# Performance work log

Hardware: AMD Instinct MI355X
Metric: run time of the kernel (lower is better)

## Reference

```python
import jax, jax.numpy as jnp
import numpy as np

N = 50000      # nodes
E = 800000     # edges (avg degree 16)
NF = 128       # input feature dim
H = 128        # hidden dim
GAMMA = 1.0    # gm init arg
COS_EPS = 1e-8 # F.cosine_similarity eps
EW_MIN = 1e-4  # edge-weight clamp


def setup_inputs() -> dict:
    key = jax.random.key(0)
    ks = jax.random.split(key, 9)
    x = jax.random.normal(ks[0], (N, NF), dtype=jnp.float32)
    edge_index = jax.random.randint(ks[1], (2, E), 0, N, dtype=jnp.int64)
    sensitive_attr = jax.random.randint(ks[2], (N,), 0, 2, dtype=jnp.int64)
    s1 = 1.0 / np.sqrt(NF)
    s2 = 1.0 / np.sqrt(H)
    W1 = jax.random.normal(ks[3], (NF, H), dtype=jnp.float32) * s1
    b1 = jnp.zeros((H,), dtype=jnp.float32)
    W2 = jax.random.normal(ks[4], (H, H), dtype=jnp.float32) * s2
    b2 = jnp.zeros((H,), dtype=jnp.float32)
    Wc = jax.random.normal(ks[5], (H, 1), dtype=jnp.float32) * s2
    bc = jnp.zeros((1,), dtype=jnp.float32)
    return {"x": x, "edge_index": edge_index, "sensitive_attr": sensitive_attr,
            "W1": W1, "b1": b1, "W2": W2, "b2": b2, "Wc": Wc, "bc": bc}


def gcn_conv(x, W, b, src, dst, ew, n):
    """PyG GCNConv: lin -> symmetric-normalized edge-weighted aggregation (+self loops) -> bias."""
    xt = x @ W                                              # [N,H]
    deg = jax.ops.segment_sum(ew, dst, num_segments=n) + 1.0  # self-loop weight 1
    dinv = jnp.where(deg > 0, deg ** -0.5, 0.0)             # [N]
    norm = dinv[src] * ew * dinv[dst]                       # [E]
    agg = jax.ops.segment_sum(xt[src] * norm[:, None], dst, num_segments=n)
    # self-loop contribution: norm_ii = dinv[i] * 1 * dinv[i]
    return agg + xt * (dinv * dinv)[:, None] + b


def reference(x, edge_index, sensitive_attr, W1, b1, W2, b2, Wc, bc):
    src, dst = edge_index[0], edge_index[1]
    # cosine-similarity edge weights (gather-heavy)
    xs, xd = x[src], x[dst]                                  # [E,F] each
    dot = jnp.sum(xs * xd, axis=1)
    ns = jnp.maximum(jnp.sqrt(jnp.sum(xs * xs, axis=1)), COS_EPS)
    nd = jnp.maximum(jnp.sqrt(jnp.sum(xd * xd, axis=1)), COS_EPS)
    sim = dot / (ns * nd)
    sen_diff = (sensitive_attr[src] != sensitive_attr[dst]).astype(x.dtype)
    ew = jnp.maximum(sim * jnp.exp(-GAMMA * sen_diff), EW_MIN)
    # two GCN layers (dropout is identity in eval mode)
    h = jax.nn.relu(gcn_conv(x, W1, b1, src, dst, ew, N))
    h = jax.nn.relu(gcn_conv(h, W2, b2, src, dst, ew, N))
    y = h @ Wc + bc                                          # [N,1]
    return (y, h)
```

## Files before the change

kernel.cpp:

```cpp
#include <hip/hip_runtime.h>


typedef unsigned short u16;
typedef unsigned int u32;
typedef __attribute__((ext_vector_type(8))) short short8;
typedef __attribute__((ext_vector_type(4))) float floatx4;

__device__ __forceinline__ float bflo(u32 u){ return __uint_as_float(u << 16); }
__device__ __forceinline__ float bfhi(u32 u){ return __uint_as_float(u & 0xFFFF0000u); }
__device__ __forceinline__ float bf1(u16 u){ return __uint_as_float(((u32)u) << 16); }
__device__ __forceinline__ u16 f2bf(float f){
    u32 u = __float_as_uint(f);
    u += 0x7FFFu + ((u >> 16) & 1u);
    return (u16)(u >> 16);
}
__device__ __forceinline__ u32 pack2(float a, float b){
    return (u32)f2bf(a) | ((u32)f2bf(b) << 16);
}
__device__ __forceinline__ float wsum(float v){
#pragma unroll
    for (int o = 32; o > 0; o >>= 1) v += __shfl_xor(v, o, 64);
    return v;
}
__device__ __forceinline__ float ld1(const void* p, size_t idx, int f32){
    return f32 ? ((const float*)p)[idx] : bf1(((const u16*)p)[idx]);
}
__device__ __forceinline__ int ldidx(const int* p, size_t i, int i64){
    return i64 ? p[2 * i] : p[i];
}

__global__ void classify_k(const u32* __restrict__ xw, const int* __restrict__ eiw,
                           int* __restrict__ flags)
{
    __shared__ int c_out, c_nz;
    int t = threadIdx.x;
    if (t == 0) { c_out = 0; c_nz = 0; }
    __syncthreads();
    u32 w = xw[t];
    int e = (w >> 7) & 0xFF;
    int outl = (e < 110 || e > 140) ? 1 : 0;
    int nz = (eiw[2 * t + 1] != 0) ? 1 : 0;
    atomicAdd(&c_out, outl);
    atomicAdd(&c_nz, nz);
    __syncthreads();
    if (t == 0) { flags[0] = (c_out > 256); flags[1] = (c_nz < 256); }
}

__global__ __launch_bounds__(256) void convhist_k(const void* __restrict__ x,
                                                  u32* __restrict__ xb,
                                                  float* __restrict__ rn, int N,
                                                  const int* __restrict__ ei,
                                                  const int* __restrict__ sa,
                                                  int* __restrict__ cnt, int E,
                                                  const void* __restrict__ W1,
                                                  const void* __restrict__ W2,
                                                  uint4* __restrict__ wf1,
                                                  uint4* __restrict__ wf2,
                                                  const int* __restrict__ flags,
                                                  int nbN, int nbE)
{
    int b = blockIdx.x;
    if (b < nbN) {
        int i = b * 4 + (threadIdx.x >> 6);
        if (i >= N) return;
        int lane = threadIdx.x & 63;
        u32 u;
        if (flags[0]) {
            const float* q = (const float*)x + (size_t)i * 128 + lane * 2;
            u = pack2(q[0], q[1]);
        } else u = ((const u32*)x)[(size_t)i * 64 + lane];
        xb[(size_t)i * 64 + lane] = u;
        float f0 = bflo(u), f1 = bfhi(u);
        float ss = wsum(f0 * f0 + f1 * f1);
        if (lane == 0) {
            float r = 1.0f / fmaxf(sqrtf(ss), 1e-8f);
            int a = flags[1] ? sa[2 * (size_t)i] : sa[i];
            rn[i] = a ? -r : r;
        }
    } else if (b < nbN + nbE) {
        int e = (b - nbN) * 256 + threadIdx.x;
        if (e >= E) return;
        int d = ldidx(ei, (size_t)E + e, flags[1]);
        if ((u32)d >= (u32)N) d = 0;
        atomicAdd(&cnt[d], 1);
    } else {
        int slot = (b - nbN - nbE) * 256 + threadIdx.x;
        if (slot >= 4096) return;
        int f32w = flags[0];
        const void* W = (slot < 2048) ? W1 : W2;
        uint4* wf = (slot < 2048) ? wf1 : wf2;
        int s = slot & 2047;
        int lane = s & 63, kk = (s >> 6) & 3, ct = s >> 8;
        int q = lane >> 4, n = lane & 15;
        int col = ct * 16 + n, k0 = kk * 32 + q * 8;
        union { u16 us[8]; uint4 u4; } tmp;
#pragma unroll
        for (int j = 0; j < 8; ++j)
            tmp.us[j] = f2bf(ld1(W, (size_t)(k0 + j) * 128 + col, f32w));
        wf[s] = tmp.u4;
    }
}

__global__ __launch_bounds__(256) void scanA_k(int* __restrict__ cnt,
                                               int* __restrict__ rowp,
                                               int* __restrict__ bsum, int N)
{
    __shared__ int wtot[4];
    int t = threadIdx.x, lane = t & 63, w = t >> 6;
    int i0 = blockIdx.x * 1024 + t * 4;
    int v[4];
#pragma unroll
    for (int k = 0; k < 4; ++k) {
        int i = i0 + k;
        v[k] = (i < N) ? cnt[i] : 0;
        if (i < N) cnt[i] = 0;
    }
    int t4 = v[0] + v[1] + v[2] + v[3];
    int sc = t4;
#pragma unroll
    for (int o = 1; o < 64; o <<= 1) {
        int nv = __shfl_up(sc, o);
        if (lane >= o) sc += nv;
    }
    if (lane == 63) wtot[w] = sc;
    __syncthreads();
    int wo = 0, tot = 0;
#pragma unroll
    for (int k = 0; k < 4; ++k) { int s = wtot[k]; if (k < w) wo += s; tot += s; }
    int pre = wo + sc - t4;
#pragma unroll
    for (int k = 0; k < 4; ++k) {
        int i = i0 + k;
        if (i < N) rowp[i] = pre;
        pre += v[k];
    }
    if (t == 0) bsum[blockIdx.x] = tot;
}

__global__ void scanB_k(int* __restrict__ bsum, int* __restrict__ rowp,
                        int nb, int N)
{
    int lane = threadIdx.x;
    int carry = 0;
    for (int base = 0; base < nb; base += 64) {
        int i = base + lane;
        int v = (i < nb) ? bsum[i] : 0;
        int sc = v;
#pragma unroll
        for (int o = 1; o < 64; o <<= 1) {
            int nv = __shfl_up(sc, o);
            if (lane >= o) sc += nv;
        }
        if (i < nb) bsum[i] = carry + sc - v;
        carry += __shfl(sc, 63);
    }
    if (lane == 0) rowp[N] = carry;
}

__global__ __launch_bounds__(256) void scanC_k(int* __restrict__ rowp,
                                               const int* __restrict__ bsum, int N)
{
    int off = bsum[blockIdx.x];
    int i0 = blockIdx.x * 1024 + threadIdx.x * 4;
#pragma unroll
    for (int k = 0; k < 4; ++k) {
        int i = i0 + k;
        if (i < N) rowp[i] += off;
    }
}

__global__ __launch_bounds__(256) void ewscat_k(const u32* __restrict__ xb,
                                                const float* __restrict__ rn,
                                                const int* __restrict__ ei,
                                                const int* __restrict__ rowp,
                                                int* __restrict__ cnt,
                                                u32* __restrict__ rec,
                                                int E, int N,
                                                const int* __restrict__ flags)
{
    int t = threadIdx.x;
    int lane = t & 63, wave = t >> 6;
    int g = lane >> 4, j = lane & 15;
    int wid = blockIdx.x * 4 + wave;
    int e0 = wid * 8 + g, e1 = e0 + 4;
    int i64 = flags[1];
    int s0 = 0, d0 = 0, s1 = 0, d1 = 0;
    bool ok0 = e0 < E, ok1 = e1 < E;
    if (ok0) {
        s0 = ldidx(ei, e0, i64); d0 = ldidx(ei, (size_t)E + e0, i64);
        if ((u32)s0 >= (u32)N) s0 = 0;
        if ((u32)d0 >= (u32)N) d0 = 0;
    }
    if (ok1) {
        s1 = ldidx(ei, e1, i64); d1 = ldidx(ei, (size_t)E + e1, i64);
        if ((u32)s1 >= (u32)N) s1 = 0;
        if ((u32)d1 >= (u32)N) d1 = 0;
    }
    uint4 A0 = ((const uint4*)(xb + (size_t)s0 * 64))[j];
    uint4 B0 = ((const uint4*)(xb + (size_t)d0 * 64))[j];
    uint4 A1 = ((const uint4*)(xb + (size_t)s1 * 64))[j];
    uint4 B1 = ((const uint4*)(xb + (size_t)d1 * 64))[j];
    float dot0 = bflo(A0.x) * bflo(B0.x) + bfhi(A0.x) * bfhi(B0.x)
               + bflo(A0.y) * bflo(B0.y) + bfhi(A0.y) * bfhi(B0.y)
               + bflo(A0.z) * bflo(B0.z) + bfhi(A0.z) * bfhi(B0.z)
               + bflo(A0.w) * bflo(B0.w) + bfhi(A0.w) * bfhi(B0.w);
    float dot1 = bflo(A1.x) * bflo(B1.x) + bfhi(A1.x) * bfhi(B1.x)
               + bflo(A1.y) * bflo(B1.y) + bfhi(A1.y) * bfhi(B1.y)
               + bflo(A1.z) * bflo(B1.z) + bfhi(A1.z) * bfhi(B1.z)
               + bflo(A1.w) * bflo(B1.w) + bfhi(A1.w) * bfhi(B1.w);
#pragma unroll
    for (int o = 8; o > 0; o >>= 1) {
        dot0 += __shfl_xor(dot0, o);
        dot1 += __shfl_xor(dot1, o);
    }
    if (j == 0) {
        if (ok0) {
            float prod = rn[s0] * rn[d0];
            float sim = dot0 * fabsf(prod);
            float f = (prod < 0.0f) ? 0.36787944117144233f : 1.0f;
            float w = fmaxf(sim * f, 1e-4f);
            int pos = rowp[d0] + atomicAdd(&cnt[d0], 1);
            if ((u32)pos >= (u32)E) pos = 0;
            rec[pos] = ((u32)s0 << 16) | f2bf(w);
        }
        if (ok1) {
            float prod = rn[s1] * rn[d1];
            float sim = dot1 * fabsf(prod);
            float f = (prod < 0.0f) ? 0.36787944117144233f : 1.0f;
            float w = fmaxf(sim * f, 1e-4f);
            int pos = rowp[d1] + atomicAdd(&cnt[d1], 1);
            if ((u32)pos >= (u32)E) pos = 0;
            rec[pos] = ((u32)s1 << 16) | f2bf(w);
        }
    }
}

__global__ __launch_bounds__(256) void dinv_k(const int* __restrict__ rowp,
                                              const u32* __restrict__ rec,
                                              float* __restrict__ dv, int N, int E)
{
    int i = blockIdx.x * 256 + threadIdx.x;
    if (i >= N) return;
    int p0 = rowp[i], p1 = rowp[i + 1];
    if (p0 < 0) p0 = 0;
    if (p1 > E) p1 = E;
    float s = 1.0f;
    for (int p = p0; p < p1; ++p) s += bf1((u16)rec[p]);
    dv[i] = 1.0f / sqrtf(s);
}

__global__ __launch_bounds__(256) void agg_k(const u32* __restrict__ feat,
                                             const int* __restrict__ rowp,
                                             const u32* __restrict__ rec,
                                             const float* __restrict__ dinv,
                                             u32* __restrict__ Tb, int N, int E)
{
    int i = blockIdx.x * 4 + (threadIdx.x >> 6);
    if (i >= N) return;
    int lane = threadIdx.x & 63;
    float di = dinv[i], sc = di * di;
    u32 u = feat[(size_t)i * 64 + lane];
    float a0 = bflo(u) * sc, a1 = bfhi(u) * sc;
    int p0 = rowp[i], p1 = rowp[i + 1];
    if (p0 < 0) p0 = 0;
    if (p1 > E) p1 = E;
    int p = p0;
    for (; p + 7 < p1; p += 8) {
        u32 r[8]; int s[8]; u32 v[8];
#pragma unroll
        for (int k = 0; k < 8; ++k) {
            r[k] = rec[p + k];
            s[k] = r[k] >> 16;
            if (s[k] >= N) s[k] = 0;
        }
#pragma unroll
        for (int k = 0; k < 8; ++k) v[k] = feat[(size_t)s[k] * 64 + lane];
#pragma unroll
        for (int k = 0; k < 8; ++k) {
            float w = bf1((u16)r[k]) * di * dinv[s[k]];
            a0 = fmaf(w, bflo(v[k]), a0);
            a1 = fmaf(w, bfhi(v[k]), a1);
        }
    }
    for (; p + 1 < p1; p += 2) {
        u32 r0 = rec[p], r1 = rec[p + 1];
        int s0 = r0 >> 16, s1 = r1 >> 16;
        if (s0 >= N) s0 = 0;
        if (s1 >= N) s1 = 0;
        u32 v0 = feat[(size_t)s0 * 64 + lane];
        u32 v1 = feat[(size_t)s1 * 64 + lane];
        float w0 = bf1((u16)r0) * di * dinv[s0];
        float w1 = bf1((u16)r1) * di * dinv[s1];
        a0 = fmaf(w0, bflo(v0), a0); a1 = fmaf(w0, bfhi(v0), a1);
        a0 = fmaf(w1, bflo(v1), a0); a1 = fmaf(w1, bfhi(v1), a1);
    }
    if (p < p1) {
        u32 r0 = rec[p];
        int s0 = r0 >> 16;
        if (s0 >= N) s0 = 0;
        u32 v0 = feat[(size_t)s0 * 64 + lane];
        float w0 = bf1((u16)r0) * di * dinv[s0];
        a0 = fmaf(w0, bflo(v0), a0); a1 = fmaf(w0, bfhi(v0), a1);
    }
    Tb[(size_t)i * 64 + lane] = pack2(a0, a1);
}

__global__ __launch_bounds__(256) void gemm_m(const u32* __restrict__ Tb,
                                              const uint4* __restrict__ wfrag,
                                              const void* __restrict__ bias,
                                              void* __restrict__ out, int outbf,
                                              int N,
                                              const void* __restrict__ Wc,
                                              const void* __restrict__ bc,
                                              float* __restrict__ yout,
                                              const int* __restrict__ flags)
{
    int t = threadIdx.x, wave = t >> 6, lane = t & 63;
    int q = lane >> 4, n = lane & 15;
    int f32w = flags[0];
    int rowbase = blockIdx.x * 64 + wave * 16;
    int arow = rowbase + n; if (arow > N - 1) arow = N - 1;
    const uint4* ap = (const uint4*)(Tb + (size_t)arow * 64);
    short8 a[4];
#pragma unroll
    for (int kk = 0; kk < 4; ++kk) {
        uint4 av = ap[kk * 4 + q];
        a[kk] = *(short8*)&av;
    }
    floatx4 acc[8];
#pragma unroll
    for (int ct = 0; ct < 8; ++ct) acc[ct] = (floatx4){0.f, 0.f, 0.f, 0.f};
#pragma unroll
    for (int ct = 0; ct < 8; ++ct) {
#pragma unroll
        for (int kk = 0; kk < 4; ++kk) {
            uint4 bv = wfrag[(ct * 4 + kk) * 64 + lane];
            acc[ct] = __builtin_amdgcn_mfma_f32_16x16x32_bf16(
                a[kk], *(short8*)&bv, acc[ct], 0, 0, 0);
        }
    }
    float bcv = 0.0f;
    float part[4] = {0.f, 0.f, 0.f, 0.f};
    if (yout) bcv = ld1(bc, 0, f32w);
#pragma unroll
    for (int ct = 0; ct < 8; ++ct) {
        int col = ct * 16 + n;
        float bia = ld1(bias, col, f32w);
        float wcv = yout ? ld1(Wc, col, f32w) : 0.0f;
#pragma unroll
        for (int r = 0; r < 4; ++r) {
            int row = rowbase + q * 4 + r;
            float h = fmaxf(acc[ct][r] + bia, 0.0f);
            if (row < N) {
                if (outbf) ((u16*)out)[(size_t)row * 128 + col] = f2bf(h);
                else       ((float*)out)[(size_t)row * 128 + col] = h;
            }
            part[r] = fmaf(h, wcv, part[r]);
        }
    }
    if (yout) {
#pragma unroll
        for (int r = 0; r < 4; ++r) {
            float pr = part[r];
#pragma unroll
            for (int o = 8; o > 0; o >>= 1) pr += __shfl_xor(pr, o);
            int row = rowbase + q * 4 + r;
            if (n == 0 && row < N) yout[row] = pr + bcv;
        }
    }
}

extern "C" void kernel_launch(void* const* d_in, const int* in_sizes, int n_in,
                              void* d_out, int out_size, void* d_ws, size_t ws_size,
                              hipStream_t stream)
{
    const void* x  = d_in[0];
    const int* ei  = (const int*)d_in[1];
    const int* sa  = (const int*)d_in[2];
    const void* W1 = d_in[3];
    const void* b1 = d_in[4];
    const void* W2 = d_in[5];
    const void* b2 = d_in[6];
    const void* Wc = d_in[7];
    const void* bc = d_in[8];
    const int N = in_sizes[2];
    const int E = in_sizes[1] / 2;

    float* y_out = (float*)d_out;
    float* h_out = y_out + N;
    u32*   Tbuf  = (u32*)d_in[0];

    const int nbN = (N + 3) / 4, nbE = (E + 255) / 256;
    const int nbS = (N + 1023) / 1024;

    char* p = (char*)d_ws;
    auto carve = [&](size_t bytes) { char* r = p; p += (bytes + 255) & ~(size_t)255; return r; };
    int*   flags = (int*)carve(256);
    float* rn    = (float*)carve((size_t)N * 4);
    float* dinv  = (float*)carve((size_t)N * 4);
    int*   cnt   = (int*)carve((size_t)N * 4);
    int*   rowp  = (int*)carve((size_t)(N + 1) * 4);
    int*   bsum  = (int*)carve((size_t)nbS * 4);
    uint4* wf1   = (uint4*)carve(2048 * 16);
    uint4* wf2   = (uint4*)carve(2048 * 16);
    u32*   rec   = (u32*)carve((size_t)E * 4);
    u32*   xb    = (u32*)carve((size_t)N * 64 * 4);

    classify_k<<<1, 1024, 0, stream>>>((const u32*)x, ei, flags);
    hipMemsetAsync(cnt, 0, (size_t)N * 4, stream);
    convhist_k<<<nbN + nbE + 16, 256, 0, stream>>>(x, xb, rn, N, ei, sa, cnt, E,
                                                   W1, W2, wf1, wf2, flags,
                                                   nbN, nbE);
    scanA_k<<<nbS, 256, 0, stream>>>(cnt, rowp, bsum, N);
    scanB_k<<<1, 64, 0, stream>>>(bsum, rowp, nbS, N);
    scanC_k<<<nbS, 256, 0, stream>>>(rowp, bsum, N);
    ewscat_k<<<(E + 31) / 32, 256, 0, stream>>>(xb, rn, ei, rowp, cnt,
                                                rec, E, N, flags);
    dinv_k<<<(N + 255) / 256, 256, 0, stream>>>(rowp, rec, dinv, N, E);

    agg_k<<<(N + 3) / 4, 256, 0, stream>>>(xb, rowp, rec, dinv, Tbuf, N, E);
    gemm_m<<<(N + 63) / 64, 256, 0, stream>>>(Tbuf, wf1, b1, xb, 1, N,
                                              nullptr, nullptr, nullptr, flags);
    agg_k<<<(N + 3) / 4, 256, 0, stream>>>(xb, rowp, rec, dinv, Tbuf, N, E);
    gemm_m<<<(N + 63) / 64, 256, 0, stream>>>(Tbuf, wf2, b2, h_out, 0, N,
                                              Wc, bc, y_out, flags);
}
```

Before: 312.9 us.

## Split scatter from edge-weight compute; compute cosine weights per destination in CSR order

The old edge-parallel kernel gathered both source and destination feature rows for every edge and then scattered into the CSR. Now a light kernel scatters only the source indices into CSR slots. A per-node kernel then loads the destination row once, computes the cosine weights for all incoming edges, writes the packed records in place, and accumulates the degree, which folds the separate dinv kernel into it. This halves the gathered feature traffic and reuses the destination row, at the cost of one extra pass over rec and load imbalance across nodes of different degree.

```diff
diff --git a/kernel.cpp b/kernel.cpp
--- a/kernel.cpp
+++ b/kernel.cpp
@@ -169,84 +169,96 @@
     }
 }
 
-__global__ __launch_bounds__(256) void ewscat_k(const u32* __restrict__ xb,
-                                                const float* __restrict__ rn,
-                                                const int* __restrict__ ei,
-                                                const int* __restrict__ rowp,
-                                                int* __restrict__ cnt,
-                                                u32* __restrict__ rec,
-                                                int E, int N,
-                                                const int* __restrict__ flags)
-{
-    int t = threadIdx.x;
-    int lane = t & 63, wave = t >> 6;
-    int g = lane >> 4, j = lane & 15;
-    int wid = blockIdx.x * 4 + wave;
-    int e0 = wid * 8 + g, e1 = e0 + 4;
+__global__ __launch_bounds__(256) void scat_k(const int* __restrict__ ei,
+                                              const int* __restrict__ rowp,
+                                              int* __restrict__ cnt,
+                                              u32* __restrict__ rec,
+                                              int E, int N,
+                                              const int* __restrict__ flags)
+{
+    int e = blockIdx.x * 256 + threadIdx.x;
+    if (e >= E) return;
     int i64 = flags[1];
-    int s0 = 0, d0 = 0, s1 = 0, d1 = 0;
-    bool ok0 = e0 < E, ok1 = e1 < E;
-    if (ok0) {
-        s0 = ldidx(ei, e0, i64); d0 = ldidx(ei, (size_t)E + e0, i64);
-        if ((u32)s0 >= (u32)N) s0 = 0;
-        if ((u32)d0 >= (u32)N) d0 = 0;
-    }
-    if (ok1) {
-        s1 = ldidx(ei, e1, i64); d1 = ldidx(ei, (size_t)E + e1, i64);
-        if ((u32)s1 >= (u32)N) s1 = 0;
-        if ((u32)d1 >= (u32)N) d1 = 0;
-    }
-    uint4 A0 = ((const uint4*)(xb + (size_t)s0 * 64))[j];
-    uint4 B0 = ((const uint4*)(xb + (size_t)d0 * 64))[j];
-    uint4 A1 = ((const uint4*)(xb + (size_t)s1 * 64))[j];
-    uint4 B1 = ((const uint4*)(xb + (size_t)d1 * 64))[j];
-    float dot0 = bflo(A0.x) * bflo(B0.x) + bfhi(A0.x) * bfhi(B0.x)
-               + bflo(A0.y) * bflo(B0.y) + bfhi(A0.y) * bfhi(B0.y)
-               + bflo(A0.z) * bflo(B0.z) + bfhi(A0.z) * bfhi(B0.z)
-               + bflo(A0.w) * bflo(B0.w) + bfhi(A0.w) * bfhi(B0.w);
-    float dot1 = bflo(A1.x) * bflo(B1.x) + bfhi(A1.x) * bfhi(B1.x)
-               + bflo(A1.y) * bflo(B1.y) + bfhi(A1.y) * bfhi(B1.y)
-               + bflo(A1.z) * bflo(B1.z) + bfhi(A1.z) * bfhi(B1.z)
-               + bflo(A1.w) * bflo(B1.w) + bfhi(A1.w) * bfhi(B1.w);
-#pragma unroll
-    for (int o = 8; o > 0; o >>= 1) {
-        dot0 += __shfl_xor(dot0, o);
-        dot1 += __shfl_xor(dot1, o);
-    }
-    if (j == 0) {
-        if (ok0) {
-            float prod = rn[s0] * rn[d0];
-            float sim = dot0 * fabsf(prod);
-            float f = (prod < 0.0f) ? 0.36787944117144233f : 1.0f;
-            float w = fmaxf(sim * f, 1e-4f);
-            int pos = rowp[d0] + atomicAdd(&cnt[d0], 1);
-            if ((u32)pos >= (u32)E) pos = 0;
-            rec[pos] = ((u32)s0 << 16) | f2bf(w);
-        }
-        if (ok1) {
-            float prod = rn[s1] * rn[d1];
-            float sim = dot1 * fabsf(prod);
-            float f = (prod < 0.0f) ? 0.36787944117144233f : 1.0f;
-            float w = fmaxf(sim * f, 1e-4f);
-            int pos = rowp[d1] + atomicAdd(&cnt[d1], 1);
-            if ((u32)pos >= (u32)E) pos = 0;
-            rec[pos] = ((u32)s1 << 16) | f2bf(w);
-        }
-    }
-}
-
-__global__ __launch_bounds__(256) void dinv_k(const int* __restrict__ rowp,
-                                              const u32* __restrict__ rec,
-                                              float* __restrict__ dv, int N, int E)
-{
-    int i = blockIdx.x * 256 + threadIdx.x;
+    int s = ldidx(ei, e, i64);
+    int d = ldidx(ei, (size_t)E + e, i64);
+    if ((u32)s >= (u32)N) s = 0;
+    if ((u32)d >= (u32)N) d = 0;
+    int pos = rowp[d] + atomicAdd(&cnt[d], 1);
+    if ((u32)pos >= (u32)E) pos = 0;
+    rec[pos] = (u32)s;
+}
+
+__global__ __launch_bounds__(256) void ewcsr_k(const u32* __restrict__ xb,
+                                               const float* __restrict__ rn,
+                                               const int* __restrict__ rowp,
+                                               u32* __restrict__ rec,
+                                               float* __restrict__ dv,
+                                               int N, int E)
+{
+    int i = blockIdx.x * 4 + (threadIdx.x >> 6);
     if (i >= N) return;
+    int lane = threadIdx.x & 63, g = lane >> 4, j = lane & 15;
+    uint4 D = ((const uint4*)(xb + (size_t)i * 64))[j];
+    float rni = rn[i];
     int p0 = rowp[i], p1 = rowp[i + 1];
     if (p0 < 0) p0 = 0;
     if (p1 > E) p1 = E;
-    float s = 1.0f;
-    for (int p = p0; p < p1; ++p) s += bf1((u16)rec[p]);
-    dv[i] = 1.0f / sqrtf(s);
+    float acc = 0.0f;
+    int p = p0 + g;
+    for (; p + 4 < p1; p += 8) {
+        int s0 = (int)rec[p];     if ((u32)s0 >= (u32)N) s0 = 0;
+        int s1 = (int)rec[p + 4]; if ((u32)s1 >= (u32)N) s1 = 0;
+        uint4 A0 = ((const uint4*)(xb + (size_t)s0 * 64))[j];
+        uint4 A1 = ((const uint4*)(xb + (size_t)s1 * 64))[j];
+        float d0 = bflo(A0.x) * bflo(D.x) + bfhi(A0.x) * bfhi(D.x)
+                 + bflo(A0.y) * bflo(D.y) + bfhi(A0.y) * bfhi(D.y)
+                 + bflo(A0.z) * bflo(D.z) + bfhi(A0.z) * bfhi(D.z)
+                 + bflo(A0.w) * bflo(D.w) + bfhi(A0.w) * bfhi(D.w);
+        float d1 = bflo(A1.x) * bflo(D.x) + bfhi(A1.x) * bfhi(D.x)
+                 + bflo(A1.y) * bflo(D.y) + bfhi(A1.y) * bfhi(D.y)
+                 + bflo(A1.z) * bflo(D.z) + bfhi(A1.z) * bfhi(D.z)
+                 + bflo(A1.w) * bflo(D.w) + bfhi(A1.w) * bfhi(D.w);
+#pragma unroll
+        for (int o = 8; o > 0; o >>= 1) {
+            d0 += __shfl_xor(d0, o);
+            d1 += __shfl_xor(d1, o);
+        }
+        if (j == 0) {
+            float pr0 = rn[s0] * rni;
+            float w0 = fmaxf(d0 * fabsf(pr0) *
+                             ((pr0 < 0.0f) ? 0.36787944117144233f : 1.0f), 1e-4f);
+            u16 wb0 = f2bf(w0);
+            rec[p] = ((u32)s0 << 16) | wb0;
+            acc += bf1(wb0);
+            float pr1 = rn[s1] * rni;
+            float w1 = fmaxf(d1 * fabsf(pr1) *
+                             ((pr1 < 0.0f) ? 0.36787944117144233f : 1.0f), 1e-4f);
+            u16 wb1 = f2bf(w1);
+            rec[p + 4] = ((u32)s1 << 16) | wb1;
+            acc += bf1(wb1);
+        }
+    }
+    if (p < p1) {
+        int s0 = (int)rec[p]; if ((u32)s0 >= (u32)N) s0 = 0;
+        uint4 A0 = ((const uint4*)(xb + (size_t)s0 * 64))[j];
+        float d0 = bflo(A0.x) * bflo(D.x) + bfhi(A0.x) * bfhi(D.x)
+                 + bflo(A0.y) * bflo(D.y) + bfhi(A0.y) * bfhi(D.y)
+                 + bflo(A0.z) * bflo(D.z) + bfhi(A0.z) * bfhi(D.z)
+                 + bflo(A0.w) * bflo(D.w) + bfhi(A0.w) * bfhi(D.w);
+#pragma unroll
+        for (int o = 8; o > 0; o >>= 1) d0 += __shfl_xor(d0, o);
+        if (j == 0) {
+            float pr0 = rn[s0] * rni;
+            float w0 = fmaxf(d0 * fabsf(pr0) *
+                             ((pr0 < 0.0f) ? 0.36787944117144233f : 1.0f), 1e-4f);
+            u16 wb0 = f2bf(w0);
+            rec[p] = ((u32)s0 << 16) | wb0;
+            acc += bf1(wb0);
+        }
+    }
+    acc += __shfl_xor(acc, 16);
+    acc += __shfl_xor(acc, 32);
+    if (lane == 0) dv[i] = 1.0f / sqrtf(1.0f + acc);
 }
 
 __global__ __launch_bounds__(256) void agg_k(const u32* __restrict__ feat,
@@ -414,9 +426,8 @@
     scanA_k<<<nbS, 256, 0, stream>>>(cnt, rowp, bsum, N);
     scanB_k<<<1, 64, 0, stream>>>(bsum, rowp, nbS, N);
     scanC_k<<<nbS, 256, 0, stream>>>(rowp, bsum, N);
-    ewscat_k<<<(E + 31) / 32, 256, 0, stream>>>(xb, rn, ei, rowp, cnt,
-                                                rec, E, N, flags);
-    dinv_k<<<(N + 255) / 256, 256, 0, stream>>>(rowp, rec, dinv, N, E);
+    scat_k<<<(E + 255) / 256, 256, 0, stream>>>(ei, rowp, cnt, rec, E, N, flags);
+    ewcsr_k<<<(N + 3) / 4, 256, 0, stream>>>(xb, rn, rowp, rec, dinv, N, E);
 
     agg_k<<<(N + 3) / 4, 256, 0, stream>>>(xb, rowp, rec, dinv, Tbuf, N, E);
     gemm_m<<<(N + 63) / 64, 256, 0, stream>>>(Tbuf, wf1, b1, xb, 1, N,
```

New measurement: 329.5 us. 1.05x slower.
